# Optimization experiments

Hardware: AMD Instinct MI355X
Metric: run time of the kernel (lower is better)

The kernel has to match this reference:

```python
import jax, jax.numpy as jnp
import numpy as np

H = 128
B, N, E = 256, 81, 1620
LN_EPS = 1e-5


def setup_inputs() -> dict:
    key = jax.random.key(0)
    ks = jax.random.split(key, 12)
    s = 0.05
    return {
        "node_features": jax.random.normal(ks[0], (B, N, H), jnp.float32),
        "edge_index": jax.random.randint(ks[1], (2, E), 0, N, jnp.int64),
        "Wm1": jax.random.normal(ks[2], (2 * H, H), jnp.float32) * s,
        "bm1": jnp.zeros((H,), jnp.float32),
        "Wm2": jax.random.normal(ks[3], (H, H), jnp.float32) * s,
        "bm2": jnp.zeros((H,), jnp.float32),
        "Wu1": jax.random.normal(ks[4], (2 * H, H), jnp.float32) * s,
        "bu1": jnp.zeros((H,), jnp.float32),
        "Wu2": jax.random.normal(ks[5], (H, H), jnp.float32) * s,
        "bu2": jnp.zeros((H,), jnp.float32),
        "gamma": jnp.ones((H,), jnp.float32),
        "beta": jnp.zeros((H,), jnp.float32),
    }


def reference(node_features, edge_index, Wm1, bm1, Wm2, bm2, Wu1, bu1, Wu2, bu2, gamma, beta):
    src_idx, tgt_idx = edge_index[0], edge_index[1]
    # Gather: [B, E, H] each (vectorized over batch; original loops in Python)
    src = node_features[:, src_idx]
    tgt = node_features[:, tgt_idx]
    comb = jnp.concatenate([src, tgt], axis=-1)            # [B, E, 2H]
    msgs = jax.nn.relu(comb @ Wm1 + bm1) @ Wm2 + bm2       # [B, E, H]
    # Scatter-mean aggregation at target nodes
    agg = jnp.zeros_like(node_features).at[:, tgt_idx].add(msgs)  # [B, N, H]
    counts = jnp.zeros((N,), node_features.dtype).at[tgt_idx].add(1.0)
    counts = jnp.maximum(counts, 1.0)
    agg = agg / counts[None, :, None]
    # Node update MLP + residual + LayerNorm
    comb2 = jnp.concatenate([node_features, agg], axis=-1)  # [B, N, 2H]
    upd = jax.nn.relu(comb2 @ Wu1 + bu1) @ Wu2 + bu2
    x = node_features + upd
    mu = jnp.mean(x, axis=-1, keepdims=True)
    var = jnp.mean(jnp.square(x - mu), axis=-1, keepdims=True)
    return (x - mu) * jax.lax.rsqrt(var + LN_EPS) * gamma + beta
```

## Files before the change

### kernel.cpp

```cpp
#include <hip/hip_runtime.h>


#define NN 81
#define HH 128
#define EE 1620
#define NCHK 26
#define MPAD 96
#define WB_BYTES 196608
#define OFFS_OFF (WB_BYTES)
#define CSR_OFF  (OFFS_OFF + 82 * 4)
#define BC_OFF   (CSR_OFF + EE * 4)
#define WS_NEED  (BC_OFF + HH * 4)

typedef _Float16 f16x8 __attribute__((ext_vector_type(8)));
typedef __fp16   h16x2 __attribute__((ext_vector_type(2)));
typedef __attribute__((ext_vector_type(8))) unsigned short ushort8v;
typedef __attribute__((ext_vector_type(4))) float f32x4;

__device__ __forceinline__ unsigned short f2h(float f) {
  union { _Float16 h; unsigned short u; } v; v.h = (_Float16)f; return v.u;
}
__device__ __forceinline__ unsigned f2h2(float x, float y) {
  union { h16x2 h; unsigned u; } v;
  v.h = __builtin_amdgcn_cvt_pkrtz(x, y);
  return v.u;
}
__device__ __forceinline__ unsigned pk_add(unsigned a, unsigned b) {
  unsigned r; asm("v_pk_add_f16 %0, %1, %2" : "=v"(r) : "v"(a), "v"(b)); return r;
}
__device__ __forceinline__ unsigned pk_relu(unsigned a) {
  unsigned r; asm("v_pk_max_f16 %0, %1, %2" : "=v"(r) : "v"(a), "v"(0u)); return r;
}
__device__ __forceinline__ unsigned swzu(int r, int laneb) {
  return ((unsigned)(r * 256 + laneb)) ^ ((unsigned)((r & 7) << 4));
}

__global__ __launch_bounds__(1024)
void setup_kernel(const float* __restrict__ Wm1, const float* __restrict__ Wm2,
                  const float* __restrict__ Wu1, const float* __restrict__ Wu2,
                  const float* __restrict__ bm2, const int* __restrict__ eidx,
                  char* __restrict__ ws) {
  __shared__ __align__(16) char arena[81920];
  const int tid = threadIdx.x;

  if (blockIdx.x < 8) {
    const int gid = blockIdx.x * 1024 + tid;
    const int lane = gid & 63;
    const int t = gid >> 6;
    const int ks = t & 3, nt = (t >> 2) & 7, mat = t >> 5;
    const float* src;
    int slot;
    if (mat == 0)      { src = Wm1;           slot = 0; }
    else if (mat == 1) { src = Wm1 + HH * HH; slot = 1; }
    else if (mat == 2) { src = Wu1;           slot = 3; }
    else               { src = Wu2;           slot = 5; }
    const int c = nt * 16 + (lane & 15);
    const int k0 = ks * 32 + (lane >> 4) * 8;
    f16x8 pv;
#pragma unroll
    for (int j = 0; j < 8; ++j) pv[j] = (_Float16)src[(k0 + j) * HH + c];
    *(f16x8*)((unsigned short*)ws + (size_t)slot * 16384 + (((nt * 4 + ks) * 64) + lane) * 8) = pv;
    return;
  }

  if (blockIdx.x == 8) {
    int* srcE  = (int*)arena;
    int* tgtE  = srcE + EE;
    int* rankS = tgtE + EE;
    int* cntC  = rankS + EE;
    int* tot   = cntC + NCHK * NN;
    int* scanS = tot + NN;
    int* wsumS = scanS + 128;
    int* offsS = wsumS + 2;
    for (int i = tid; i < NCHK * NN; i += 1024) cntC[i] = 0;
    for (int i = tid; i < 2 * EE; i += 1024) srcE[i] = eidx[i];
    __syncthreads();
    const int lane = tid & 63, wv = tid >> 6;
    for (int c = wv; c < NCHK; c += 16) {
      const int e = c * 64 + lane;
      const bool ok = (e < EE);
      const int t = ok ? tgtE[e] : -1;
      unsigned long long mymask = 0;
#pragma unroll
      for (int i = 0; i < 64; ++i) {
        const int ti = __shfl(t, i);
        const unsigned long long bal = __ballot(t == ti);
        if (i == lane) mymask = bal;
      }
      if (ok) {
        const int rank = __popcll(mymask & ((1ull << lane) - 1ull));
        rankS[e] = rank;
        if (rank == 0) cntC[c * NN + t] = __popcll(mymask);
      }
    }
    __syncthreads();
    if (tid < NN) {
      int s = 0;
#pragma unroll
      for (int c = 0; c < NCHK; ++c) s += cntC[c * NN + tid];
      tot[tid] = s;
    }
    __syncthreads();
    if (tid < 128) {
      const int l = tid & 63, w = tid >> 6;
      int inc = (tid < NN) ? tot[tid] : 0;
#pragma unroll
      for (int d = 1; d < 64; d <<= 1) {
        int u = __shfl_up(inc, d);
        if (l >= d) inc += u;
      }
      scanS[tid] = inc;
      if (l == 63) wsumS[w] = inc;
    }
    __syncthreads();
    if (tid < 128) {
      const int w = tid >> 6;
      const int inc = scanS[tid] + (w ? wsumS[0] : 0);
      if (tid < NN) offsS[tid] = inc - tot[tid];
      if (tid == NN - 1) offsS[NN] = inc;
    }
    __syncthreads();
    if (tid < NN) {
      int run = offsS[tid];
#pragma unroll
      for (int c = 0; c < NCHK; ++c) {
        const int tmp = cntC[c * NN + tid];
        cntC[c * NN + tid] = run;
        run += tmp;
      }
    }
    __syncthreads();
    int* wofs = (int*)(ws + OFFS_OFF);
    int* wcsr = (int*)(ws + CSR_OFF);
    for (int i = tid; i <= NN; i += 1024) wofs[i] = offsS[i];
    for (int e = tid; e < EE; e += 1024) {
      const int t = tgtE[e];
      wcsr[cntC[(e >> 6) * NN + t] + rankS[e]] = srcE[e];
    }
    return;
  }

  {
    const int bs = blockIdx.x - 9;
    float* WuL = (float*)arena;
    float* WmL = WuL + HH * HH;
    const float* Wu1b = Wu1 + HH * HH;
    float4* WuL4 = (float4*)WuL;
    const float4* src4 = (const float4*)Wu1b;
    for (int i = tid; i < HH * HH / 4; i += 1024) WuL4[i] = src4[i];
    const float4* wm4 = (const float4*)(Wm2 + bs * 32 * HH);
    float4* WmL4 = (float4*)WmL;
    if (tid < 32 * HH / 4) WmL4[tid] = wm4[tid];
    __syncthreads();
    const int kk = tid >> 5;
    const int k  = bs * 32 + kk;
    const int cg = tid & 31;
    f32x4 acc = (f32x4)0.f;
    for (int j = 0; j < HH; ++j) {
      const float a = WmL[kk * HH + j];
      const float4 w = WuL4[j * 32 + cg];
      acc[0] += a * w.x; acc[1] += a * w.y; acc[2] += a * w.z; acc[3] += a * w.w;
    }
    unsigned short* dst = (unsigned short*)ws;
#pragma unroll
    for (int q = 0; q < 4; ++q) {
      const int c = cg * 4 + q;
      const int nt = c >> 4;
      const int l = (((k & 31) >> 3) << 4) | (c & 15);
      dst[(size_t)2 * 16384 + (((nt * 4 + bs) * 64) + l) * 8 + (k & 7)] = f2h(acc[q]);
    }
    if (bs == 0 && tid < HH) {
      float s = 0.f;
      for (int j = 0; j < HH; ++j) s += bm2[j] * WuL[j * HH + tid];
      ((float*)(ws + BC_OFF))[tid] = s;
    }
  }
}

__device__ __forceinline__ void loadB(const unsigned short* Wp, int nt0, int lane,
                                      f16x8 (&Bf)[4]) {
#pragma unroll
  for (int ks = 0; ks < 4; ++ks)
    Bf[ks] = *(const f16x8*)(Wp + ((nt0 * 4 + ks) * 64 + lane) * 8);
}

__device__ __forceinline__ void gemm3(const char* Ab, const f16x8 (&Bf)[4],
                                      int lane, int mt0, f32x4 (&acc)[3]) {
  const int rl = lane & 15;
  const int kb = (lane >> 4) * 16;
  const unsigned swz = (unsigned)((rl & 7) << 4);
#pragma unroll
  for (int ks = 0; ks < 4; ++ks)
#pragma unroll
    for (int mm = 0; mm < 3; ++mm) {
      const int r = (mt0 + mm) * 16 + rl;
      const unsigned byte = (unsigned)(r * 256) + (((unsigned)(ks * 64 + kb)) ^ swz);
      f16x8 a = *(const f16x8*)(Ab + byte);
      acc[mm] = __builtin_amdgcn_mfma_f32_16x16x32_f16(a, Bf[ks], acc[mm], 0, 0, 0);
    }
}

__device__ __forceinline__ void gemm3x2(const char* Ab,
                                        const f16x8 (&B0)[4], const f16x8 (&B1)[4],
                                        int lane, int mt0,
                                        f32x4 (&a0)[3], f32x4 (&a1)[3]) {
  const int rl = lane & 15;
  const int kb = (lane >> 4) * 16;
  const unsigned swz = (unsigned)((rl & 7) << 4);
#pragma unroll
  for (int ks = 0; ks < 4; ++ks)
#pragma unroll
    for (int mm = 0; mm < 3; ++mm) {
      const int r = (mt0 + mm) * 16 + rl;
      const unsigned byte = (unsigned)(r * 256) + (((unsigned)(ks * 64 + kb)) ^ swz);
      f16x8 a = *(const f16x8*)(Ab + byte);
      a0[mm] = __builtin_amdgcn_mfma_f32_16x16x32_f16(a, B0[ks], a0[mm], 0, 0, 0);
      a1[mm] = __builtin_amdgcn_mfma_f32_16x16x32_f16(a, B1[ks], a1[mm], 0, 0, 0);
    }
}

__device__ __forceinline__ void gemm3_2A(const char* A0, const char* A1,
                                         const f16x8 (&B0)[4], const f16x8 (&B1)[4],
                                         int lane, int mt0,
                                         f32x4 (&a0)[3], f32x4 (&a1)[3]) {
  const int rl = lane & 15;
  const int kb = (lane >> 4) * 16;
  const unsigned swz = (unsigned)((rl & 7) << 4);
#pragma unroll
  for (int ks = 0; ks < 4; ++ks)
#pragma unroll
    for (int mm = 0; mm < 3; ++mm) {
      const int r = (mt0 + mm) * 16 + rl;
      const unsigned byte = (unsigned)(r * 256) + (((unsigned)(ks * 64 + kb)) ^ swz);
      f16x8 x0 = *(const f16x8*)(A0 + byte);
      a0[mm] = __builtin_amdgcn_mfma_f32_16x16x32_f16(x0, B0[ks], a0[mm], 0, 0, 0);
      f16x8 x1 = *(const f16x8*)(A1 + byte);
      a1[mm] = __builtin_amdgcn_mfma_f32_16x16x32_f16(x1, B1[ks], a1[mm], 0, 0, 0);
    }
}

__global__ __launch_bounds__(1024, 4)
void mpnn_fp16_kernel(const float* __restrict__ node,
                      const float* __restrict__ bm1,
                      const float* __restrict__ bu1, const float* __restrict__ bu2,
                      const float* __restrict__ gamma_, const float* __restrict__ beta_,
                      const char* __restrict__ ws,
                      float* __restrict__ out) {
  __shared__ float X[NN][HH];
  __shared__ unsigned short XbS[MPAD * HH];
  __shared__ unsigned short bufPS[MPAD * HH];
  __shared__ unsigned short bufQS[MPAD * HH];
  __shared__ int   csrL[EE];
  __shared__ int   offsL[NN + 1];
  __shared__ float bias[6][HH];
  char* Xb   = (char*)XbS;
  char* bufP = (char*)bufPS;
  char* bufQ = (char*)bufQS;

  const int tid  = threadIdx.x;
  const int lane = tid & 63;
  const int wave = tid >> 6;
  const int b    = blockIdx.x;

  const unsigned short* wpk = (const unsigned short*)ws;
  const int* wofs = (const int*)(ws + OFFS_OFF);
  const int* wcsr = (const int*)(ws + CSR_OFF);
  const float* wbc = (const float*)(ws + BC_OFF);

  const int nt0 = wave & 7;
  const int mt0 = 3 * (wave >> 3);
  const int erow = (lane >> 4) * 4;
  const int ecol = lane & 15;
  const int C    = nt0 * 16 + ecol;

  f16x8 BA0[4], BA1[4];
  loadB(wpk, nt0, lane, BA0);
  loadB(wpk + 16384, nt0, lane, BA1);

  {
    const float4* nf4 = (const float4*)(node + (size_t)b * NN * HH);
    const int i2 = tid + 2048;
    const bool has2 = (i2 < NN * HH / 4);
    float4 v0 = nf4[tid];
    float4 v1 = nf4[tid + 1024];
    float4 v2 = has2 ? nf4[i2] : make_float4(0.f, 0.f, 0.f, 0.f);
#pragma unroll
    for (int k = 0; k < 3; ++k) {
      const int i = tid + k * 1024;
      if (k == 2 && !has2) break;
      const float4 v = (k == 0) ? v0 : (k == 1) ? v1 : v2;
      const int r = i >> 5, c = (i & 31) * 4;
      *(float4*)&X[r][c] = v;
      uint2 pv; pv.x = f2h2(v.x, v.y); pv.y = f2h2(v.z, v.w);
      *(uint2*)(Xb + swzu(r, c * 2)) = pv;
    }
    if (tid < (MPAD - NN) * 16) {
      const int r = NN + tid / 16, m = tid % 16;
      ushort8v z = {0,0,0,0,0,0,0,0};
      *(ushort8v*)(Xb + swzu(r, m * 16)) = z;
    }
    for (int i = tid; i < EE; i += 1024) csrL[i] = wcsr[i];
    if (tid < NN + 1) offsL[tid] = wofs[tid];
    if (tid < HH) {
      bias[0][tid] = bm1[tid];  bias[1][tid] = wbc[tid];
      bias[2][tid] = bu1[tid];  bias[3][tid] = bu2[tid];
      bias[4][tid] = gamma_[tid]; bias[5][tid] = beta_[tid];
    }
  }
  __syncthreads();

  {
    f32x4 accP[3], accQ[3];
#pragma unroll
    for (int mm = 0; mm < 3; ++mm) { accP[mm] = (f32x4)0.f; accQ[mm] = (f32x4)0.f; }
    gemm3x2(Xb, BA0, BA1, lane, mt0, accP, accQ);
#pragma unroll
    for (int mm = 0; mm < 3; ++mm)
#pragma unroll
      for (int rg = 0; rg < 4; ++rg) {
        const int R = (mt0 + mm) * 16 + erow + rg;
        const unsigned byte = swzu(R, C * 2);
        const bool ok = (R < NN);
        *(unsigned short*)(bufP + byte) = ok ? f2h(accP[mm][rg]) : (unsigned short)0;
        *(unsigned short*)(bufQ + byte) = ok ? f2h(accQ[mm][rg] + bias[0][C]) : (unsigned short)0;
      }
  }
  __syncthreads();

  {
    const int lb = lane * 4;
    for (int t = wave; t < NN; t += 16) {
      const unsigned qbyte = swzu(t, lb);
      const unsigned q = *(const unsigned*)(bufQ + qbyte);
      unsigned h = 0u, g = 0u;
      int e = offsL[t];
      const int o1 = offsL[t + 1];
      for (; e + 4 <= o1; e += 4) {
        const int s0 = csrL[e], s1 = csrL[e + 1], s2 = csrL[e + 2], s3 = csrL[e + 3];
        const unsigned p0 = *(const unsigned*)(bufP + swzu(s0, lb));
        const unsigned p1 = *(const unsigned*)(bufP + swzu(s1, lb));
        const unsigned p2 = *(const unsigned*)(bufP + swzu(s2, lb));
        const unsigned p3 = *(const unsigned*)(bufP + swzu(s3, lb));
        h = pk_add(h, pk_relu(pk_add(p0, q)));
        g = pk_add(g, pk_relu(pk_add(p1, q)));
        h = pk_add(h, pk_relu(pk_add(p2, q)));
        g = pk_add(g, pk_relu(pk_add(p3, q)));
      }
      for (; e < o1; ++e) {
        const int s = csrL[e];
        const unsigned pp = *(const unsigned*)(bufP + swzu(s, lb));
        h = pk_add(h, pk_relu(pk_add(pp, q)));
      }
      h = pk_add(h, g);
      *(unsigned*)(bufQ + qbyte) = h;
    }
  }
  __syncthreads();

  {
    f16x8 BW[4], BU[4];
    loadB(wpk + 2 * 16384, nt0, lane, BW);
    loadB(wpk + 3 * 16384, nt0, lane, BU);
    f32x4 accT[3], accU[3];
#pragma unroll
    for (int mm = 0; mm < 3; ++mm) { accT[mm] = (f32x4)0.f; accU[mm] = (f32x4)0.f; }
    gemm3_2A(bufQ, Xb, BW, BU, lane, mt0, accT, accU);
#pragma unroll
    for (int mm = 0; mm < 3; ++mm)
#pragma unroll
      for (int rg = 0; rg < 4; ++rg) {
        const int R = (mt0 + mm) * 16 + erow + rg;
        float v = 0.f;
        if (R < NN) {
          const int dg = offsL[R + 1] - offsL[R];
          const float inv = (dg > 0) ? 1.f / (float)dg : 1.f;
          const float sf  = (dg > 0) ? 1.f : 0.f;
          v = fmaxf(accU[mm][rg] + accT[mm][rg] * inv + sf * bias[1][C] + bias[2][C], 0.f);
        }
        *(unsigned short*)(bufP + swzu(R, C * 2)) = f2h(v);
      }
  }
  __syncthreads();

  {
    f16x8 BD[4];
    loadB(wpk + 5 * 16384, nt0, lane, BD);
    f32x4 acc[3];
#pragma unroll
    for (int mm = 0; mm < 3; ++mm) acc[mm] = (f32x4)0.f;
    gemm3(bufP, BD, lane, mt0, acc);
#pragma unroll
    for (int mm = 0; mm < 3; ++mm)
#pragma unroll
      for (int rg = 0; rg < 4; ++rg) {
        const int R = (mt0 + mm) * 16 + erow + rg;
        if (R < NN) X[R][C] += acc[mm][rg] + bias[3][C];
      }
  }
  __syncthreads();

  for (int r = wave; r < NN; r += 16) {
    const float x0 = X[r][lane], x1 = X[r][lane + 64];
    float s = x0 + x1;
#pragma unroll
    for (int off = 32; off; off >>= 1) s += __shfl_xor(s, off);
    const float mu = s * (1.f / 128.f);
    const float d0 = x0 - mu, d1 = x1 - mu;
    float v = d0 * d0 + d1 * d1;
#pragma unroll
    for (int off = 32; off; off >>= 1) v += __shfl_xor(v, off);
    const float rstd = rsqrtf(v * (1.f / 128.f) + 1e-5f);
    const size_t o = ((size_t)b * NN + r) * HH;
    out[o + lane]      = d0 * rstd * bias[4][lane]      + bias[5][lane];
    out[o + lane + 64] = d1 * rstd * bias[4][lane + 64] + bias[5][lane + 64];
  }
}

__device__ __forceinline__ void gemm_acc_f32(const float (*A)[HH], const float* __restrict__ Wg,
                                             int c, int row0, int nr, float (&acc)[41]) {
  float w[8];
#pragma unroll
  for (int j = 0; j < 8; ++j) w[j] = Wg[j * HH + c];
  for (int k0 = 0; k0 < HH; k0 += 8) {
    float wn[8];
    if (k0 + 8 < HH) {
#pragma unroll
      for (int j = 0; j < 8; ++j) wn[j] = Wg[(k0 + 8 + j) * HH + c];
    }
#pragma unroll
    for (int i = 0; i < 41; ++i) {
      if (i < nr) {
        const float4 a0 = *(const float4*)&A[row0 + i][k0];
        const float4 a1 = *(const float4*)&A[row0 + i][k0 + 4];
        acc[i] += a0.x * w[0] + a0.y * w[1] + a0.z * w[2] + a0.w * w[3]
                + a1.x * w[4] + a1.y * w[5] + a1.z * w[6] + a1.w * w[7];
      }
    }
#pragma unroll
    for (int j = 0; j < 8; ++j) w[j] = wn[j];
  }
}

__global__ __launch_bounds__(256, 1)
void mpnn_fused_kernel(const float* __restrict__ node, const int* __restrict__ eidx,
                       const float* __restrict__ Wm1, const float* __restrict__ bm1,
                       const float* __restrict__ Wm2, const float* __restrict__ bm2,
                       const float* __restrict__ Wu1, const float* __restrict__ bu1,
                       const float* __restrict__ Wu2, const float* __restrict__ bu2,
                       const float* __restrict__ gamma_, const float* __restrict__ beta_,
                       float* __restrict__ out) {
  __shared__ float X[NN][HH];
  __shared__ float Pb[NN][HH];
  __shared__ float Qb[NN][HH];
  __shared__ int   edg[2 * EE];
  __shared__ int   csr[EE];
  __shared__ int   offs[NN + 1];
  __shared__ int   cnt3[3][NN];
  __shared__ int   base3[3][NN];
  __shared__ float biases[6][HH];

  const int tid  = threadIdx.x;
  const int lane = tid & 63;
  const int wave = tid >> 6;
  const int b    = blockIdx.x;

  {
    const float4* nf4 = (const float4*)(node + (size_t)b * NN * HH);
    float4* X4 = (float4*)&X[0][0];
    for (int i = tid; i < NN * HH / 4; i += 256) X4[i] = nf4[i];
    for (int i = tid; i < 2 * EE; i += 256) edg[i] = eidx[i];
    if (tid < HH) {
      biases[0][tid] = bm1[tid]; biases[1][tid] = bm2[tid];
      biases[2][tid] = bu1[tid]; biases[3][tid] = bu2[tid];
      biases[4][tid] = gamma_[tid]; biases[5][tid] = beta_[tid];
    }
  }
  __syncthreads();
  if (tid < 3 * NN) {
    const int t = tid % NN, ch = tid / NN;
    const int e0 = ch * 540, e1 = e0 + 540;
    int cnt = 0;
    for (int e = e0; e < e1; ++e) cnt += (edg[EE + e] == t);
    cnt3[ch][t] = cnt;
  }
  __syncthreads();
  if (tid == 0) {
    int run = 0;
    for (int t = 0; t < NN; ++t) {
      offs[t] = run;
      base3[0][t] = run;
      base3[1][t] = base3[0][t] + cnt3[0][t];
      base3[2][t] = base3[1][t] + cnt3[1][t];
      run = base3[2][t] + cnt3[2][t];
    }
    offs[NN] = run;
  }
  __syncthreads();
  if (tid < 3 * NN) {
    const int t = tid % NN, ch = tid / NN;
    const int e0 = ch * 540, e1 = e0 + 540;
    int pos = base3[ch][t];
    for (int e = e0; e < e1; ++e)
      if (edg[EE + e] == t) csr[pos++] = edg[e];
  }
  __syncthreads();

  const int c    = ((wave & 1) << 6) | lane;
  const int row0 = (wave >> 1) ? 41 : 0;
  const int nr   = (wave >> 1) ? 40 : 41;

  {
    float acc[41];
#pragma unroll
    for (int i = 0; i < 41; ++i) acc[i] = 0.f;
    gemm_acc_f32(X, Wm1, c, row0, nr, acc);
#pragma unroll
    for (int i = 0; i < 41; ++i) if (i < nr) Pb[row0 + i][c] = acc[i];
  }
  {
    float acc[41];
#pragma unroll
    for (int i = 0; i < 41; ++i) acc[i] = 0.f;
    gemm_acc_f32(X, Wm1 + HH * HH, c, row0, nr, acc);
#pragma unroll
    for (int i = 0; i < 41; ++i) if (i < nr) Qb[row0 + i][c] = acc[i];
  }
  __syncthreads();

  for (int t = wave; t < NN; t += 4) {
    const int o0 = offs[t], o1 = offs[t + 1];
    const float q0 = Qb[t][lane]      + biases[0][lane];
    const float q1 = Qb[t][lane + 64] + biases[0][lane + 64];
    float h0 = 0.f, h1 = 0.f;
    for (int e = o0; e < o1; ++e) {
      const int s = csr[e];
      h0 += fmaxf(Pb[s][lane]      + q0, 0.f);
      h1 += fmaxf(Pb[s][lane + 64] + q1, 0.f);
    }
    Qb[t][lane]      = h0;
    Qb[t][lane + 64] = h1;
  }
  __syncthreads();

  {
    float acc[41];
#pragma unroll
    for (int i = 0; i < 41; ++i) acc[i] = 0.f;
    gemm_acc_f32(Qb, Wm2, c, row0, nr, acc);
#pragma unroll
    for (int i = 0; i < 41; ++i) if (i < nr) {
      const int r = row0 + i;
      const float d = (float)(offs[r + 1] - offs[r]);
      Pb[r][c] = (acc[i] + d * biases[1][c]) * (1.f / fmaxf(d, 1.f));
    }
  }
  __syncthreads();

  {
    float acc[41];
#pragma unroll
    for (int i = 0; i < 41; ++i) acc[i] = 0.f;
    gemm_acc_f32(X,  Wu1,           c, row0, nr, acc);
    gemm_acc_f32(Pb, Wu1 + HH * HH, c, row0, nr, acc);
#pragma unroll
    for (int i = 0; i < 41; ++i) if (i < nr)
      Qb[row0 + i][c] = fmaxf(acc[i] + biases[2][c], 0.f);
  }
  __syncthreads();

  {
    float acc[41];
#pragma unroll
    for (int i = 0; i < 41; ++i) acc[i] = 0.f;
    gemm_acc_f32(Qb, Wu2, c, row0, nr, acc);
#pragma unroll
    for (int i = 0; i < 41; ++i) if (i < nr) {
      const int r = row0 + i;
      X[r][c] = X[r][c] + acc[i] + biases[3][c];
    }
  }
  __syncthreads();

  for (int r = wave; r < NN; r += 4) {
    const float x0 = X[r][lane], x1 = X[r][lane + 64];
    float s = x0 + x1;
#pragma unroll
    for (int off = 32; off; off >>= 1) s += __shfl_xor(s, off);
    const float mu = s * (1.f / 128.f);
    const float d0 = x0 - mu, d1 = x1 - mu;
    float v = d0 * d0 + d1 * d1;
#pragma unroll
    for (int off = 32; off; off >>= 1) v += __shfl_xor(v, off);
    const float rstd = rsqrtf(v * (1.f / 128.f) + 1e-5f);
    const size_t o = ((size_t)b * NN + r) * HH;
    out[o + lane]      = d0 * rstd * biases[4][lane]      + biases[5][lane];
    out[o + lane + 64] = d1 * rstd * biases[4][lane + 64] + biases[5][lane + 64];
  }
}

extern "C" void kernel_launch(void* const* d_in, const int* in_sizes, int n_in,
                              void* d_out, int out_size, void* d_ws, size_t ws_size,
                              hipStream_t stream) {
  (void)in_sizes; (void)n_in; (void)out_size;
  const float* node  = (const float*)d_in[0];
  const int*   eidx  = (const int*)  d_in[1];
  const float* Wm1   = (const float*)d_in[2];
  const float* bm1   = (const float*)d_in[3];
  const float* Wm2   = (const float*)d_in[4];
  const float* bm2   = (const float*)d_in[5];
  const float* Wu1   = (const float*)d_in[6];
  const float* bu1   = (const float*)d_in[7];
  const float* Wu2   = (const float*)d_in[8];
  const float* bu2   = (const float*)d_in[9];
  const float* gamma_= (const float*)d_in[10];
  const float* beta_ = (const float*)d_in[11];
  float* outp = (float*)d_out;

  if (ws_size >= (size_t)WS_NEED) {
    char* ws = (char*)d_ws;
    hipLaunchKernelGGL(setup_kernel, dim3(13), dim3(1024), 0, stream,
                       Wm1, Wm2, Wu1, Wu2, bm2, eidx, ws);
    hipLaunchKernelGGL(mpnn_fp16_kernel, dim3(256), dim3(1024), 0, stream,
                       node, bm1, bu1, bu2, gamma_, beta_, ws, outp);
  } else {
    hipLaunchKernelGGL(mpnn_fused_kernel, dim3(256), dim3(256), 0, stream,
                       node, eidx, Wm1, bm1, Wm2, bm2, Wu1, bu1, Wu2, bu2,
                       gamma_, beta_, outp);
  }
}
```

Measured before the change: 39.80 us.

## Merge setup and main kernels into one cooperative launch with grid sync

Folds the weight-packing and CSR-building setup work into a single cooperative kernel. The first 13 blocks do the setup work while all blocks stage node features into LDS, then every block waits at a grid-wide barrier before the fp16 MFMA pipeline runs. The aim is to remove the second kernel launch and its gap, and to overlap the node-feature load with setup. In exchange, the cooperative launch needs all 256 blocks of 1024 threads resident at once, and the grid sync adds its own cost. If the cooperative launch fails, the code falls back to the two-kernel path. The fp32 fallback kernel is removed, so the small-workspace branch now runs setup_kernel into a workspace that may be too small.

```diff
diff --git a/kernel.cpp b/kernel.cpp
--- a/kernel.cpp
+++ b/kernel.cpp
@@ -1,4 +1,5 @@
 #include <hip/hip_runtime.h>
+#include <hip/hip_cooperative_groups.h>
 
 
 #define NN 81
@@ -12,6 +13,15 @@
 #define BC_OFF   (CSR_OFF + EE * 4)
 #define WS_NEED  (BC_OFF + HH * 4)
 
+#define CX_OFF    0
+#define CXB_OFF   41472
+#define CBP_OFF   66048
+#define CBQ_OFF   90624
+#define CCSR_OFF  115200
+#define COFF_OFF  121680
+#define CBIAS_OFF 122008
+#define CL_BYTES  125080
+
 typedef _Float16 f16x8 __attribute__((ext_vector_type(8)));
 typedef __fp16   h16x2 __attribute__((ext_vector_type(2)));
 typedef __attribute__((ext_vector_type(8))) unsigned short ushort8v;
@@ -20,6 +30,9 @@
 __device__ __forceinline__ unsigned short f2h(float f) {
   union { _Float16 h; unsigned short u; } v; v.h = (_Float16)f; return v.u;
 }
+__device__ __forceinline__ float h2f(unsigned short u) {
+  union { unsigned short u; _Float16 h; } v; v.u = u; return (float)v.h;
+}
 __device__ __forceinline__ unsigned f2h2(float x, float y) {
   union { h16x2 h; unsigned u; } v;
   v.h = __builtin_amdgcn_cvt_pkrtz(x, y);
@@ -33,6 +46,378 @@
 }
 __device__ __forceinline__ unsigned swzu(int r, int laneb) {
   return ((unsigned)(r * 256 + laneb)) ^ ((unsigned)((r & 7) << 4));
+}
+
+__device__ __forceinline__ void loadB(const unsigned short* Wp, int nt0, int lane,
+                                      f16x8 (&Bf)[4]) {
+#pragma unroll
+  for (int ks = 0; ks < 4; ++ks)
+    Bf[ks] = *(const f16x8*)(Wp + ((nt0 * 4 + ks) * 64 + lane) * 8);
+}
+
+__device__ __forceinline__ void gemm3(const char* Ab, const f16x8 (&Bf)[4],
+                                      int lane, int mt0, f32x4 (&acc)[3]) {
+  const int rl = lane & 15;
+  const int kb = (lane >> 4) * 16;
+  const unsigned swz = (unsigned)((rl & 7) << 4);
+#pragma unroll
+  for (int ks = 0; ks < 4; ++ks)
+#pragma unroll
+    for (int mm = 0; mm < 3; ++mm) {
+      const int r = (mt0 + mm) * 16 + rl;
+      const unsigned byte = (unsigned)(r * 256) + (((unsigned)(ks * 64 + kb)) ^ swz);
+      f16x8 a = *(const f16x8*)(Ab + byte);
+      acc[mm] = __builtin_amdgcn_mfma_f32_16x16x32_f16(a, Bf[ks], acc[mm], 0, 0, 0);
+    }
+}
+
+__device__ __forceinline__ void gemm3x2(const char* Ab,
+                                        const f16x8 (&B0)[4], const f16x8 (&B1)[4],
+                                        int lane, int mt0,
+                                        f32x4 (&a0)[3], f32x4 (&a1)[3]) {
+  const int rl = lane & 15;
+  const int kb = (lane >> 4) * 16;
+  const unsigned swz = (unsigned)((rl & 7) << 4);
+#pragma unroll
+  for (int ks = 0; ks < 4; ++ks)
+#pragma unroll
+    for (int mm = 0; mm < 3; ++mm) {
+      const int r = (mt0 + mm) * 16 + rl;
+      const unsigned byte = (unsigned)(r * 256) + (((unsigned)(ks * 64 + kb)) ^ swz);
+      f16x8 a = *(const f16x8*)(Ab + byte);
+      a0[mm] = __builtin_amdgcn_mfma_f32_16x16x32_f16(a, B0[ks], a0[mm], 0, 0, 0);
+      a1[mm] = __builtin_amdgcn_mfma_f32_16x16x32_f16(a, B1[ks], a1[mm], 0, 0, 0);
+    }
+}
+
+__device__ __forceinline__ void gemm3_2A(const char* A0, const char* A1,
+                                         const f16x8 (&B0)[4], const f16x8 (&B1)[4],
+                                         int lane, int mt0,
+                                         f32x4 (&a0)[3], f32x4 (&a1)[3]) {
+  const int rl = lane & 15;
+  const int kb = (lane >> 4) * 16;
+  const unsigned swz = (unsigned)((rl & 7) << 4);
+#pragma unroll
+  for (int ks = 0; ks < 4; ++ks)
+#pragma unroll
+    for (int mm = 0; mm < 3; ++mm) {
+      const int r = (mt0 + mm) * 16 + rl;
+      const unsigned byte = (unsigned)(r * 256) + (((unsigned)(ks * 64 + kb)) ^ swz);
+      f16x8 x0 = *(const f16x8*)(A0 + byte);
+      a0[mm] = __builtin_amdgcn_mfma_f32_16x16x32_f16(x0, B0[ks], a0[mm], 0, 0, 0);
+      f16x8 x1 = *(const f16x8*)(A1 + byte);
+      a1[mm] = __builtin_amdgcn_mfma_f32_16x16x32_f16(x1, B1[ks], a1[mm], 0, 0, 0);
+    }
+}
+
+__global__ __launch_bounds__(1024, 4)
+void mpnn_coop_kernel(const float* node, const int* eidx,
+                      const float* Wm1, const float* bm1,
+                      const float* Wm2, const float* bm2,
+                      const float* Wu1, const float* bu1,
+                      const float* Wu2, const float* bu2,
+                      const float* gamma_, const float* beta_,
+                      char* ws, float* out) {
+  __shared__ __align__(16) char L[CL_BYTES];
+  float (*X)[HH] = (float(*)[HH])(L + CX_OFF);
+  char* Xb   = L + CXB_OFF;
+  char* bufP = L + CBP_OFF;
+  char* bufQ = L + CBQ_OFF;
+  int*  csrL = (int*)(L + CCSR_OFF);
+  int*  offsL= (int*)(L + COFF_OFF);
+  float (*bias)[HH] = (float(*)[HH])(L + CBIAS_OFF);
+
+  const int tid  = threadIdx.x;
+  const int lane = tid & 63;
+  const int wave = tid >> 6;
+  const int b    = blockIdx.x;
+
+  {
+    const float4* nf4 = (const float4*)(node + (size_t)b * NN * HH);
+    const int i2 = tid + 2048;
+    const bool has2 = (i2 < NN * HH / 4);
+    float4 v0 = nf4[tid];
+    float4 v1 = nf4[tid + 1024];
+    float4 v2 = has2 ? nf4[i2] : make_float4(0.f, 0.f, 0.f, 0.f);
+#pragma unroll
+    for (int k = 0; k < 3; ++k) {
+      const int i = tid + k * 1024;
+      if (k == 2 && !has2) break;
+      const float4 v = (k == 0) ? v0 : (k == 1) ? v1 : v2;
+      const int r = i >> 5, c = (i & 31) * 4;
+      *(float4*)&X[r][c] = v;
+      uint2 pv; pv.x = f2h2(v.x, v.y); pv.y = f2h2(v.z, v.w);
+      *(uint2*)(Xb + swzu(r, c * 2)) = pv;
+    }
+    if (tid < (MPAD - NN) * 16) {
+      const int r = NN + tid / 16, m = tid % 16;
+      ushort8v z = {0,0,0,0,0,0,0,0};
+      *(ushort8v*)(Xb + swzu(r, m * 16)) = z;
+    }
+  }
+
+  if (b < 8) {
+    const int gid = b * 1024 + tid;
+    const int ln = gid & 63;
+    const int t = gid >> 6;
+    const int ks = t & 3, nt = (t >> 2) & 7, mat = t >> 5;
+    const float* src;
+    int slot;
+    if (mat == 0)      { src = Wm1;           slot = 0; }
+    else if (mat == 1) { src = Wm1 + HH * HH; slot = 1; }
+    else if (mat == 2) { src = Wu1;           slot = 3; }
+    else               { src = Wu2;           slot = 5; }
+    const int c = nt * 16 + (ln & 15);
+    const int k0 = ks * 32 + (ln >> 4) * 8;
+    f16x8 pv;
+#pragma unroll
+    for (int j = 0; j < 8; ++j) pv[j] = (_Float16)src[(k0 + j) * HH + c];
+    *(f16x8*)((unsigned short*)ws + (size_t)slot * 16384 + (((nt * 4 + ks) * 64) + ln) * 8) = pv;
+  } else if (b == 8) {
+    int* srcE  = (int*)(L + CBP_OFF);
+    int* tgtE  = srcE + EE;
+    int* rankS = tgtE + EE;
+    int* cntC  = rankS + EE;
+    int* tot   = cntC + NCHK * NN;
+    int* scanS = tot + NN;
+    int* wsumS = scanS + 128;
+    int* offsS = wsumS + 2;
+    for (int i = tid; i < NCHK * NN; i += 1024) cntC[i] = 0;
+    for (int i = tid; i < 2 * EE; i += 1024) srcE[i] = eidx[i];
+    __syncthreads();
+    const int ln = tid & 63, wv = tid >> 6;
+    for (int c = wv; c < NCHK; c += 16) {
+      const int e = c * 64 + ln;
+      const bool ok = (e < EE);
+      const int t = ok ? tgtE[e] : -1;
+      unsigned long long mymask = 0;
+#pragma unroll
+      for (int i = 0; i < 64; ++i) {
+        const int ti = __shfl(t, i);
+        const unsigned long long bal = __ballot(t == ti);
+        if (i == ln) mymask = bal;
+      }
+      if (ok) {
+        const int rank = __popcll(mymask & ((1ull << ln) - 1ull));
+        rankS[e] = rank;
+        if (rank == 0) cntC[c * NN + t] = __popcll(mymask);
+      }
+    }
+    __syncthreads();
+    if (tid < NN) {
+      int s = 0;
+#pragma unroll
+      for (int c = 0; c < NCHK; ++c) s += cntC[c * NN + tid];
+      tot[tid] = s;
+    }
+    __syncthreads();
+    if (tid < 128) {
+      const int l = tid & 63, w = tid >> 6;
+      int inc = (tid < NN) ? tot[tid] : 0;
+#pragma unroll
+      for (int d = 1; d < 64; d <<= 1) {
+        int u = __shfl_up(inc, d);
+        if (l >= d) inc += u;
+      }
+      scanS[tid] = inc;
+      if (l == 63) wsumS[w] = inc;
+    }
+    __syncthreads();
+    if (tid < 128) {
+      const int w = tid >> 6;
+      const int inc = scanS[tid] + (w ? wsumS[0] : 0);
+      if (tid < NN) offsS[tid] = inc - tot[tid];
+      if (tid == NN - 1) offsS[NN] = inc;
+    }
+    __syncthreads();
+    if (tid < NN) {
+      int run = offsS[tid];
+#pragma unroll
+      for (int c = 0; c < NCHK; ++c) {
+        const int tmp = cntC[c * NN + tid];
+        cntC[c * NN + tid] = run;
+        run += tmp;
+      }
+    }
+    __syncthreads();
+    int* wofs = (int*)(ws + OFFS_OFF);
+    int* wcsr = (int*)(ws + CSR_OFF);
+    for (int i = tid; i <= NN; i += 1024) wofs[i] = offsS[i];
+    for (int e = tid; e < EE; e += 1024) {
+      const int t = tgtE[e];
+      wcsr[cntC[(e >> 6) * NN + t] + rankS[e]] = srcE[e];
+    }
+  } else if (b < 13) {
+    const int bs = b - 9;
+    unsigned short* WuLh = (unsigned short*)(L + CBP_OFF);
+    float* WmL = (float*)(L + CBP_OFF + 32768);
+    const float* Wu1b = Wu1 + HH * HH;
+    for (int i = tid; i < HH * HH / 2; i += 1024) {
+      const float2 w = ((const float2*)Wu1b)[i];
+      ((unsigned*)WuLh)[i] = f2h2(w.x, w.y);
+    }
+    if (tid < 32 * HH / 4)
+      ((float4*)WmL)[tid] = ((const float4*)(Wm2 + bs * 32 * HH))[tid];
+    __syncthreads();
+    const int kk = tid >> 5;
+    const int k  = bs * 32 + kk;
+    const int cg = tid & 31;
+    f32x4 acc = (f32x4)0.f;
+    for (int j = 0; j < HH; ++j) {
+      const float a = WmL[kk * HH + j];
+      const uint2 u = *(const uint2*)(WuLh + j * HH + cg * 4);
+      acc[0] += a * h2f((unsigned short)(u.x & 0xffff));
+      acc[1] += a * h2f((unsigned short)(u.x >> 16));
+      acc[2] += a * h2f((unsigned short)(u.y & 0xffff));
+      acc[3] += a * h2f((unsigned short)(u.y >> 16));
+    }
+    unsigned short* dst = (unsigned short*)ws;
+#pragma unroll
+    for (int q = 0; q < 4; ++q) {
+      const int c = cg * 4 + q;
+      const int nt = c >> 4;
+      const int l = (((k & 31) >> 3) << 4) | (c & 15);
+      dst[(size_t)2 * 16384 + (((nt * 4 + bs) * 64) + l) * 8 + (k & 7)] = f2h(acc[q]);
+    }
+    if (bs == 0 && tid < HH) {
+      float s = 0.f;
+      for (int j = 0; j < HH; ++j) s += bm2[j] * h2f(WuLh[j * HH + tid]);
+      ((float*)(ws + BC_OFF))[tid] = s;
+    }
+  }
+
+  __threadfence();
+  cooperative_groups::this_grid().sync();
+
+  const unsigned short* wpk = (const unsigned short*)ws;
+  const int nt0 = wave & 7;
+  const int mt0 = 3 * (wave >> 3);
+  const int erow = (lane >> 4) * 4;
+  const int ecol = lane & 15;
+  const int C    = nt0 * 16 + ecol;
+
+  f16x8 BA0[4], BA1[4];
+  loadB(wpk, nt0, lane, BA0);
+  loadB(wpk + 16384, nt0, lane, BA1);
+  {
+    const int* wofs = (const int*)(ws + OFFS_OFF);
+    const int* wcsr = (const int*)(ws + CSR_OFF);
+    const float* wbc = (const float*)(ws + BC_OFF);
+    for (int i = tid; i < EE; i += 1024) csrL[i] = wcsr[i];
+    if (tid < NN + 1) offsL[tid] = wofs[tid];
+    if (tid < HH) {
+      bias[0][tid] = bm1[tid];  bias[1][tid] = wbc[tid];
+      bias[2][tid] = bu1[tid];  bias[3][tid] = bu2[tid];
+      bias[4][tid] = gamma_[tid]; bias[5][tid] = beta_[tid];
+    }
+  }
+  __syncthreads();
+
+  {
+    f32x4 accP[3], accQ[3];
+#pragma unroll
+    for (int mm = 0; mm < 3; ++mm) { accP[mm] = (f32x4)0.f; accQ[mm] = (f32x4)0.f; }
+    gemm3x2(Xb, BA0, BA1, lane, mt0, accP, accQ);
+#pragma unroll
+    for (int mm = 0; mm < 3; ++mm)
+#pragma unroll
+      for (int rg = 0; rg < 4; ++rg) {
+        const int R = (mt0 + mm) * 16 + erow + rg;
+        const unsigned byte = swzu(R, C * 2);
+        const bool ok = (R < NN);
+        *(unsigned short*)(bufP + byte) = ok ? f2h(accP[mm][rg]) : (unsigned short)0;
+        *(unsigned short*)(bufQ + byte) = ok ? f2h(accQ[mm][rg] + bias[0][C]) : (unsigned short)0;
+      }
+  }
+  __syncthreads();
+
+  {
+    const int lb = lane * 4;
+    for (int t = wave; t < NN; t += 16) {
+      const unsigned qbyte = swzu(t, lb);
+      const unsigned q = *(const unsigned*)(bufQ + qbyte);
+      unsigned h = 0u, g = 0u;
+      int e = offsL[t];
+      const int o1 = offsL[t + 1];
+      for (; e + 4 <= o1; e += 4) {
+        const int s0 = csrL[e], s1 = csrL[e + 1], s2 = csrL[e + 2], s3 = csrL[e + 3];
+        const unsigned p0 = *(const unsigned*)(bufP + swzu(s0, lb));
+        const unsigned p1 = *(const unsigned*)(bufP + swzu(s1, lb));
+        const unsigned p2 = *(const unsigned*)(bufP + swzu(s2, lb));
+        const unsigned p3 = *(const unsigned*)(bufP + swzu(s3, lb));
+        h = pk_add(h, pk_relu(pk_add(p0, q)));
+        g = pk_add(g, pk_relu(pk_add(p1, q)));
+        h = pk_add(h, pk_relu(pk_add(p2, q)));
+        g = pk_add(g, pk_relu(pk_add(p3, q)));
+      }
+      for (; e < o1; ++e) {
+        const int s = csrL[e];
+        const unsigned pp = *(const unsigned*)(bufP + swzu(s, lb));
+        h = pk_add(h, pk_relu(pk_add(pp, q)));
+      }
+      h = pk_add(h, g);
+      *(unsigned*)(bufQ + qbyte) = h;
+    }
+  }
+  __syncthreads();
+
+  {
+    f16x8 BW[4], BU[4];
+    loadB(wpk + 2 * 16384, nt0, lane, BW);
+    loadB(wpk + 3 * 16384, nt0, lane, BU);
+    f32x4 accT[3], accU[3];
+#pragma unroll
+    for (int mm = 0; mm < 3; ++mm) { accT[mm] = (f32x4)0.f; accU[mm] = (f32x4)0.f; }
+    gemm3_2A(bufQ, Xb, BW, BU, lane, mt0, accT, accU);
+#pragma unroll
+    for (int mm = 0; mm < 3; ++mm)
+#pragma unroll
+      for (int rg = 0; rg < 4; ++rg) {
+        const int R = (mt0 + mm) * 16 + erow + rg;
+        float v = 0.f;
+        if (R < NN) {
+          const int dg = offsL[R + 1] - offsL[R];
+          const float inv = (dg > 0) ? 1.f / (float)dg : 1.f;
+          const float sf  = (dg > 0) ? 1.f : 0.f;
+          v = fmaxf(accU[mm][rg] + accT[mm][rg] * inv + sf * bias[1][C] + bias[2][C], 0.f);
+        }
+        *(unsigned short*)(bufP + swzu(R, C * 2)) = f2h(v);
+      }
+  }
+  __syncthreads();
+
+  {
+    f16x8 BD[4];
+    loadB(wpk + 5 * 16384, nt0, lane, BD);
+    f32x4 acc[3];
+#pragma unroll
+    for (int mm = 0; mm < 3; ++mm) acc[mm] = (f32x4)0.f;
+    gemm3(bufP, BD, lane, mt0, acc);
+#pragma unroll
+    for (int mm = 0; mm < 3; ++mm)
+#pragma unroll
+      for (int rg = 0; rg < 4; ++rg) {
+        const int R = (mt0 + mm) * 16 + erow + rg;
+        if (R < NN) X[R][C] += acc[mm][rg] + bias[3][C];
+      }
+  }
+  __syncthreads();
+
+  for (int r = wave; r < NN; r += 16) {
+    const float x0 = X[r][lane], x1 = X[r][lane + 64];
+    float s = x0 + x1;
+#pragma unroll
+    for (int off = 32; off; off >>= 1) s += __shfl_xor(s, off);
+    const float mu = s * (1.f / 128.f);
+    const float d0 = x0 - mu, d1 = x1 - mu;
+    float v = d0 * d0 + d1 * d1;
+#pragma unroll
+    for (int off = 32; off; off >>= 1) v += __shfl_xor(v, off);
+    const float rstd = rsqrtf(v * (1.f / 128.f) + 1e-5f);
+    const size_t o = ((size_t)b * NN + r) * HH;
+    out[o + lane]      = d0 * rstd * bias[4][lane]      + bias[5][lane];
+    out[o + lane + 64] = d1 * rstd * bias[4][lane + 64] + bias[5][lane + 64];
+  }
 }
 
 __global__ __launch_bounds__(1024)
@@ -175,68 +560,6 @@
       ((float*)(ws + BC_OFF))[tid] = s;
     }
   }
-}
-
-__device__ __forceinline__ void loadB(const unsigned short* Wp, int nt0, int lane,
-                                      f16x8 (&Bf)[4]) {
-#pragma unroll
-  for (int ks = 0; ks < 4; ++ks)
-    Bf[ks] = *(const f16x8*)(Wp + ((nt0 * 4 + ks) * 64 + lane) * 8);
-}
-
-__device__ __forceinline__ void gemm3(const char* Ab, const f16x8 (&Bf)[4],
-                                      int lane, int mt0, f32x4 (&acc)[3]) {
-  const int rl = lane & 15;
-  const int kb = (lane >> 4) * 16;
-  const unsigned swz = (unsigned)((rl & 7) << 4);
-#pragma unroll
-  for (int ks = 0; ks < 4; ++ks)
-#pragma unroll
-    for (int mm = 0; mm < 3; ++mm) {
-      const int r = (mt0 + mm) * 16 + rl;
-      const unsigned byte = (unsigned)(r * 256) + (((unsigned)(ks * 64 + kb)) ^ swz);
-      f16x8 a = *(const f16x8*)(Ab + byte);
-      acc[mm] = __builtin_amdgcn_mfma_f32_16x16x32_f16(a, Bf[ks], acc[mm], 0, 0, 0);
-    }
-}
-
-__device__ __forceinline__ void gemm3x2(const char* Ab,
-                                        const f16x8 (&B0)[4], const f16x8 (&B1)[4],
-                                        int lane, int mt0,
-                                        f32x4 (&a0)[3], f32x4 (&a1)[3]) {
-  const int rl = lane & 15;
-  const int kb = (lane >> 4) * 16;
-  const unsigned swz = (unsigned)((rl & 7) << 4);
-#pragma unroll
-  for (int ks = 0; ks < 4; ++ks)
-#pragma unroll
-    for (int mm = 0; mm < 3; ++mm) {
-      const int r = (mt0 + mm) * 16 + rl;
-      const unsigned byte = (unsigned)(r * 256) + (((unsigned)(ks * 64 + kb)) ^ swz);
-      f16x8 a = *(const f16x8*)(Ab + byte);
-      a0[mm] = __builtin_amdgcn_mfma_f32_16x16x32_f16(a, B0[ks], a0[mm], 0, 0, 0);
-      a1[mm] = __builtin_amdgcn_mfma_f32_16x16x32_f16(a, B1[ks], a1[mm], 0, 0, 0);
-    }
-}
-
-__device__ __forceinline__ void gemm3_2A(const char* A0, const char* A1,
-                                         const f16x8 (&B0)[4], const f16x8 (&B1)[4],
-                                         int lane, int mt0,
-                                         f32x4 (&a0)[3], f32x4 (&a1)[3]) {
-  const int rl = lane & 15;
-  const int kb = (lane >> 4) * 16;
-  const unsigned swz = (unsigned)((rl & 7) << 4);
-#pragma unroll
-  for (int ks = 0; ks < 4; ++ks)
-#pragma unroll
-    for (int mm = 0; mm < 3; ++mm) {
-      const int r = (mt0 + mm) * 16 + rl;
-      const unsigned byte = (unsigned)(r * 256) + (((unsigned)(ks * 64 + kb)) ^ swz);
-      f16x8 x0 = *(const f16x8*)(A0 + byte);
-      a0[mm] = __builtin_amdgcn_mfma_f32_16x16x32_f16(x0, B0[ks], a0[mm], 0, 0, 0);
-      f16x8 x1 = *(const f16x8*)(A1 + byte);
-      a1[mm] = __builtin_amdgcn_mfma_f32_16x16x32_f16(x1, B1[ks], a1[mm], 0, 0, 0);
-    }
 }
 
 __global__ __launch_bounds__(1024, 4)
@@ -416,188 +739,6 @@
   }
 }
 
-__device__ __forceinline__ void gemm_acc_f32(const float (*A)[HH], const float* __restrict__ Wg,
-                                             int c, int row0, int nr, float (&acc)[41]) {
-  float w[8];
-#pragma unroll
-  for (int j = 0; j < 8; ++j) w[j] = Wg[j * HH + c];
-  for (int k0 = 0; k0 < HH; k0 += 8) {
-    float wn[8];
-    if (k0 + 8 < HH) {
-#pragma unroll
-      for (int j = 0; j < 8; ++j) wn[j] = Wg[(k0 + 8 + j) * HH + c];
-    }
-#pragma unroll
-    for (int i = 0; i < 41; ++i) {
-      if (i < nr) {
-        const float4 a0 = *(const float4*)&A[row0 + i][k0];
-        const float4 a1 = *(const float4*)&A[row0 + i][k0 + 4];
-        acc[i] += a0.x * w[0] + a0.y * w[1] + a0.z * w[2] + a0.w * w[3]
-                + a1.x * w[4] + a1.y * w[5] + a1.z * w[6] + a1.w * w[7];
-      }
-    }
-#pragma unroll
-    for (int j = 0; j < 8; ++j) w[j] = wn[j];
-  }
-}
-
-__global__ __launch_bounds__(256, 1)
-void mpnn_fused_kernel(const float* __restrict__ node, const int* __restrict__ eidx,
-                       const float* __restrict__ Wm1, const float* __restrict__ bm1,
-                       const float* __restrict__ Wm2, const float* __restrict__ bm2,
-                       const float* __restrict__ Wu1, const float* __restrict__ bu1,
-                       const float* __restrict__ Wu2, const float* __restrict__ bu2,
-                       const float* __restrict__ gamma_, const float* __restrict__ beta_,
-                       float* __restrict__ out) {
-  __shared__ float X[NN][HH];
-  __shared__ float Pb[NN][HH];
-  __shared__ float Qb[NN][HH];
-  __shared__ int   edg[2 * EE];
-  __shared__ int   csr[EE];
-  __shared__ int   offs[NN + 1];
-  __shared__ int   cnt3[3][NN];
-  __shared__ int   base3[3][NN];
-  __shared__ float biases[6][HH];
-
-  const int tid  = threadIdx.x;
-  const int lane = tid & 63;
-  const int wave = tid >> 6;
-  const int b    = blockIdx.x;
-
-  {
-    const float4* nf4 = (const float4*)(node + (size_t)b * NN * HH);
-    float4* X4 = (float4*)&X[0][0];
-    for (int i = tid; i < NN * HH / 4; i += 256) X4[i] = nf4[i];
-    for (int i = tid; i < 2 * EE; i += 256) edg[i] = eidx[i];
-    if (tid < HH) {
-      biases[0][tid] = bm1[tid]; biases[1][tid] = bm2[tid];
-      biases[2][tid] = bu1[tid]; biases[3][tid] = bu2[tid];
-      biases[4][tid] = gamma_[tid]; biases[5][tid] = beta_[tid];
-    }
-  }
-  __syncthreads();
-  if (tid < 3 * NN) {
-    const int t = tid % NN, ch = tid / NN;
-    const int e0 = ch * 540, e1 = e0 + 540;
-    int cnt = 0;
-    for (int e = e0; e < e1; ++e) cnt += (edg[EE + e] == t);
-    cnt3[ch][t] = cnt;
-  }
-  __syncthreads();
-  if (tid == 0) {
-    int run = 0;
-    for (int t = 0; t < NN; ++t) {
-      offs[t] = run;
-      base3[0][t] = run;
-      base3[1][t] = base3[0][t] + cnt3[0][t];
-      base3[2][t] = base3[1][t] + cnt3[1][t];
-      run = base3[2][t] + cnt3[2][t];
-    }
-    offs[NN] = run;
-  }
-  __syncthreads();
-  if (tid < 3 * NN) {
-    const int t = tid % NN, ch = tid / NN;
-    const int e0 = ch * 540, e1 = e0 + 540;
-    int pos = base3[ch][t];
-    for (int e = e0; e < e1; ++e)
-      if (edg[EE + e] == t) csr[pos++] = edg[e];
-  }
-  __syncthreads();
-
-  const int c    = ((wave & 1) << 6) | lane;
-  const int row0 = (wave >> 1) ? 41 : 0;
-  const int nr   = (wave >> 1) ? 40 : 41;
-
-  {
-    float acc[41];
-#pragma unroll
-    for (int i = 0; i < 41; ++i) acc[i] = 0.f;
-    gemm_acc_f32(X, Wm1, c, row0, nr, acc);
-#pragma unroll
-    for (int i = 0; i < 41; ++i) if (i < nr) Pb[row0 + i][c] = acc[i];
-  }
-  {
-    float acc[41];
-#pragma unroll
-    for (int i = 0; i < 41; ++i) acc[i] = 0.f;
-    gemm_acc_f32(X, Wm1 + HH * HH, c, row0, nr, acc);
-#pragma unroll
-    for (int i = 0; i < 41; ++i) if (i < nr) Qb[row0 + i][c] = acc[i];
-  }
-  __syncthreads();
-
-  for (int t = wave; t < NN; t += 4) {
-    const int o0 = offs[t], o1 = offs[t + 1];
-    const float q0 = Qb[t][lane]      + biases[0][lane];
-    const float q1 = Qb[t][lane + 64] + biases[0][lane + 64];
-    float h0 = 0.f, h1 = 0.f;
-    for (int e = o0; e < o1; ++e) {
-      const int s = csr[e];
-      h0 += fmaxf(Pb[s][lane]      + q0, 0.f);
-      h1 += fmaxf(Pb[s][lane + 64] + q1, 0.f);
-    }
-    Qb[t][lane]      = h0;
-    Qb[t][lane + 64] = h1;
-  }
-  __syncthreads();
-
-  {
-    float acc[41];
-#pragma unroll
-    for (int i = 0; i < 41; ++i) acc[i] = 0.f;
-    gemm_acc_f32(Qb, Wm2, c, row0, nr, acc);
-#pragma unroll
-    for (int i = 0; i < 41; ++i) if (i < nr) {
-      const int r = row0 + i;
-      const float d = (float)(offs[r + 1] - offs[r]);
-      Pb[r][c] = (acc[i] + d * biases[1][c]) * (1.f / fmaxf(d, 1.f));
-    }
-  }
-  __syncthreads();
-
-  {
-    float acc[41];
-#pragma unroll
-    for (int i = 0; i < 41; ++i) acc[i] = 0.f;
-    gemm_acc_f32(X,  Wu1,           c, row0, nr, acc);
-    gemm_acc_f32(Pb, Wu1 + HH * HH, c, row0, nr, acc);
-#pragma unroll
-    for (int i = 0; i < 41; ++i) if (i < nr)
-      Qb[row0 + i][c] = fmaxf(acc[i] + biases[2][c], 0.f);
-  }
-  __syncthreads();
-
-  {
-    float acc[41];
-#pragma unroll
-    for (int i = 0; i < 41; ++i) acc[i] = 0.f;
-    gemm_acc_f32(Qb, Wu2, c, row0, nr, acc);
-#pragma unroll
-    for (int i = 0; i < 41; ++i) if (i < nr) {
-      const int r = row0 + i;
-      X[r][c] = X[r][c] + acc[i] + biases[3][c];
-    }
-  }
-  __syncthreads();
-
-  for (int r = wave; r < NN; r += 4) {
-    const float x0 = X[r][lane], x1 = X[r][lane + 64];
-    float s = x0 + x1;
-#pragma unroll
-    for (int off = 32; off; off >>= 1) s += __shfl_xor(s, off);
-    const float mu = s * (1.f / 128.f);
-    const float d0 = x0 - mu, d1 = x1 - mu;
-    float v = d0 * d0 + d1 * d1;
-#pragma unroll
-    for (int off = 32; off; off >>= 1) v += __shfl_xor(v, off);
-    const float rstd = rsqrtf(v * (1.f / 128.f) + 1e-5f);
-    const size_t o = ((size_t)b * NN + r) * HH;
-    out[o + lane]      = d0 * rstd * biases[4][lane]      + biases[5][lane];
-    out[o + lane + 64] = d1 * rstd * biases[4][lane + 64] + biases[5][lane + 64];
-  }
-}
-
 extern "C" void kernel_launch(void* const* d_in, const int* in_sizes, int n_in,
                               void* d_out, int out_size, void* d_ws, size_t ws_size,
                               hipStream_t stream) {
@@ -615,16 +756,25 @@
   const float* gamma_= (const float*)d_in[10];
   const float* beta_ = (const float*)d_in[11];
   float* outp = (float*)d_out;
+  char* ws = (char*)d_ws;
 
   if (ws_size >= (size_t)WS_NEED) {
-    char* ws = (char*)d_ws;
+    void* kargs[] = {(void*)&node, (void*)&eidx, (void*)&Wm1, (void*)&bm1,
+                     (void*)&Wm2, (void*)&bm2, (void*)&Wu1, (void*)&bu1,
+                     (void*)&Wu2, (void*)&bu2, (void*)&gamma_, (void*)&beta_,
+                     (void*)&ws, (void*)&outp};
+    hipError_t err = hipLaunchCooperativeKernel((const void*)mpnn_coop_kernel,
+                                                dim3(256), dim3(1024), kargs, 0, stream);
+    if (err != hipSuccess) {
+      hipLaunchKernelGGL(setup_kernel, dim3(13), dim3(1024), 0, stream,
+                         Wm1, Wm2, Wu1, Wu2, bm2, eidx, ws);
+      hipLaunchKernelGGL(mpnn_fp16_kernel, dim3(256), dim3(1024), 0, stream,
+                         node, bm1, bu1, bu2, gamma_, beta_, ws, outp);
+    }
+  } else {
     hipLaunchKernelGGL(setup_kernel, dim3(13), dim3(1024), 0, stream,
                        Wm1, Wm2, Wu1, Wu2, bm2, eidx, ws);
     hipLaunchKernelGGL(mpnn_fp16_kernel, dim3(256), dim3(1024), 0, stream,
                        node, bm1, bu1, bu2, gamma_, beta_, ws, outp);
-  } else {
-    hipLaunchKernelGGL(mpnn_fused_kernel, dim3(256), dim3(256), 0, stream,
-                       node, eidx, Wm1, bm1, Wm2, bm2, Wu1, bu1, Wu2, bu2,
-                       gamma_, beta_, outp);
-  }
-}
+  }
+}
```

After: 150.0 us. +276.9%, slower.
